# Kernel tuning notes

Measured on AMD Instinct MI355X. Metric: run time of the kernel, lower is better.

The kernel has to match this reference:

```python
import jax, jax.numpy as jnp
import numpy as np

B, S, D, H, DH, FF = 8, 512, 1024, 16, 64, 4096
NEG_MIN = jnp.finfo(jnp.float32).min


def setup_inputs() -> dict:
    key = jax.random.key(0)
    ks = jax.random.split(key, 12)
    sc = lambda d: d ** -0.5
    return {
        "x": jax.random.normal(ks[0], (B, S, D), jnp.float32),
        "mask": jnp.ones((B, S), jnp.float32),
        "special_attn": jax.nn.softmax(jax.random.normal(ks[1], (B, S, S), jnp.float32), axis=-1),
        "special_value": jax.random.normal(ks[2], (B, 1, S, DH), jnp.float32),
        "Wq": jax.random.normal(ks[3], (D, H * DH), jnp.float32) * sc(D),
        "bq": jnp.zeros((H * DH,), jnp.float32),
        "Wk": jax.random.normal(ks[4], (D, H * DH), jnp.float32) * sc(D),
        "bk": jnp.zeros((H * DH,), jnp.float32),
        "Wv": jax.random.normal(ks[5], (D, H * DH), jnp.float32) * sc(D),
        "bv": jnp.zeros((H * DH,), jnp.float32),
        "Wo": jax.random.normal(ks[6], ((H + 1) * DH, D), jnp.float32) * sc((H + 1) * DH),
        "bo": jnp.zeros((D,), jnp.float32),
        "ln1_g": jnp.ones((D,), jnp.float32),
        "ln1_b": jnp.zeros((D,), jnp.float32),
        "W1": jax.random.normal(ks[7], (D, FF), jnp.float32) * sc(D),
        "b1": jnp.zeros((FF,), jnp.float32),
        "W2": jax.random.normal(ks[8], (FF, D), jnp.float32) * sc(FF),
        "b2": jnp.zeros((D,), jnp.float32),
        "ln2_g": jnp.ones((D,), jnp.float32),
        "ln2_b": jnp.zeros((D,), jnp.float32),
    }


def _layer_norm(x, g, b, eps=1e-6):
    mu = jnp.mean(x, axis=-1, keepdims=True)
    var = jnp.mean(jnp.square(x - mu), axis=-1, keepdims=True)
    return (x - mu) * jax.lax.rsqrt(var + eps) * g + b


def _split_heads(t):  # [B,S,H*DH] -> [B,H,S,DH]
    return t.reshape(B, S, H, DH).transpose(0, 2, 1, 3)


def reference(x, mask, special_attn, special_value, Wq, bq, Wk, bk, Wv, bv,
              Wo, bo, ln1_g, ln1_b, W1, b1, W2, b2, ln2_g, ln2_b):
    # --- self-attention sublayer (pre-norm, residual) ---
    y = _layer_norm(x, ln1_g, ln1_b)
    q = _split_heads(y @ Wq + bq) * (DH ** -0.5)
    k = _split_heads(y @ Wk + bk)
    v = _split_heads(y @ Wv + bv)
    dot = jnp.einsum("bhqd,bhkd->bhqk", q, k)
    m = mask[:, None, None, :]  # [B,1,1,S]
    dot = dot * m + (1.0 - m) * NEG_MIN
    attn = jax.nn.softmax(dot, axis=-1)  # [B,H,S,S]
    # concat special attention map as an extra head; special values are PREPENDED
    attn = jnp.concatenate([attn, special_attn[:, None]], axis=1)   # [B,H+1,S,S]
    vals = jnp.concatenate([special_value, v], axis=1)              # [B,H+1,S,DH]
    heads = jnp.einsum("bhqk,bhkd->bhqd", attn, vals)               # [B,H+1,S,DH]
    combined = heads.transpose(0, 2, 1, 3).reshape(B, S, (H + 1) * DH)
    x = x + (combined @ Wo + bo)
    # --- FFN sublayer (pre-norm, residual, leaky_relu alpha=0.2) ---
    y = _layer_norm(x, ln2_g, ln2_b)
    h = jax.nn.leaky_relu(y @ W1 + b1, negative_slope=0.2)
    x = x + (h @ W2 + b2)
    return x
```

## Files before the change

### kernel.cpp

```cpp
#include <hip/hip_runtime.h>
#include <hip/hip_bf16.h>

#define BB 8
#define SS 512
#define DD 1024
#define HH 16
#define DHH 64
#define FFF 4096
#define MM (BB*SS)
#define HD (HH*DHH)
#define CD ((HH+1)*DHH)
#define QKV_LD 3072

#define NEG_MIN (-3.4028234663852886e38f)
#define FLT_MAX_ (3.402823466e+38f)

typedef __attribute__((ext_vector_type(8)))  __bf16 bf16x8;
typedef __attribute__((ext_vector_type(16))) float  f32x16;

__device__ __forceinline__ unsigned short bf16_rne(float x) {
    unsigned int u = __float_as_uint(x);
    u += 0x7FFFu + ((u >> 16) & 1u);
    return (unsigned short)(u >> 16);
}
__device__ __forceinline__ float bf16f(unsigned short h) {
    return __uint_as_float(((unsigned int)h) << 16);
}
__device__ __forceinline__ void split2(float x, unsigned short& h, unsigned short& l) {
    h = bf16_rne(x);
    l = bf16_rne(x - bf16f(h));
}

__global__ __launch_bounds__(256)
void ln_plane_kernel(const float* __restrict__ x, const float* __restrict__ g,
                     const float* __restrict__ bta,
                     unsigned short* __restrict__ oh, unsigned short* __restrict__ ol)
{
    const int row = blockIdx.x;
    const int tid = threadIdx.x;
    const float* xr = x + (size_t)row * DD;
    float4 xv = *(const float4*)(xr + tid * 4);
    float s  = xv.x + xv.y + xv.z + xv.w;
    float ss = xv.x*xv.x + xv.y*xv.y + xv.z*xv.z + xv.w*xv.w;
    #pragma unroll
    for (int off = 32; off > 0; off >>= 1) {
        s  += __shfl_down(s, off);
        ss += __shfl_down(ss, off);
    }
    __shared__ float red[8];
    const int wid = tid >> 6;
    if ((tid & 63) == 0) { red[wid*2] = s; red[wid*2+1] = ss; }
    __syncthreads();
    s  = red[0] + red[2] + red[4] + red[6];
    ss = red[1] + red[3] + red[5] + red[7];
    const float mu  = s * (1.0f / DD);
    const float var = ss * (1.0f / DD) - mu * mu;
    const float inv = 1.0f / sqrtf(var + 1e-6f);
    float4 gv = *(const float4*)(g + tid*4);
    float4 bv = *(const float4*)(bta + tid*4);
    float o0 = (xv.x - mu) * inv * gv.x + bv.x;
    float o1 = (xv.y - mu) * inv * gv.y + bv.y;
    float o2 = (xv.z - mu) * inv * gv.z + bv.z;
    float o3 = (xv.w - mu) * inv * gv.w + bv.w;
    ushort4 h4, l4;
    split2(o0, h4.x, l4.x); split2(o1, h4.y, l4.y);
    split2(o2, h4.z, l4.z); split2(o3, h4.w, l4.w);
    *(ushort4*)&oh[(size_t)row * DD + tid*4] = h4;
    *(ushort4*)&ol[(size_t)row * DD + tid*4] = l4;
}

template<bool QKV, bool HAS_RES, bool LEAKY, bool OUTP, int NT>
__global__ __launch_bounds__(256)
void gemm_mfma(const unsigned short* __restrict__ Ahi,
               const unsigned short* __restrict__ Alo,
               const float* __restrict__ B0, const float* __restrict__ B1,
               const float* __restrict__ B2,
               const float* __restrict__ bias0, const float* __restrict__ bias1,
               const float* __restrict__ bias2,
               const float* __restrict__ res, float* __restrict__ Cf,
               unsigned short* __restrict__ Chi, unsigned short* __restrict__ Clo,
               int K, int lda, int ldb, int ldc)
{
    static_assert(NT == 64 || NT == 128, "");
    constexpr int NF    = NT / 64;
    constexpr int BFRAG = NT / 32;
    constexpr int KG    = 256 / NT;
    constexpr int KPT   = 32 / KG;

    __shared__ unsigned short Ah[4096];
    __shared__ unsigned short Al[4096];
    __shared__ unsigned short Bh[BFRAG * 2 * 64 * 8];
    __shared__ unsigned short Bl[BFRAG * 2 * 64 * 8];

    const int tid = threadIdx.x;
    const int bm  = blockIdx.y;
    int bn = blockIdx.x;

    const float* Bw   = B0;
    const float* bias = bias0;
    float scale = 1.0f;
    if (QKV) {
        const int sel = bn >> 3;
        Bw   = (sel == 0) ? B0 : (sel == 1 ? B1 : B2);
        bias = (sel == 0) ? bias0 : (sel == 1 ? bias1 : bias2);
        scale = (sel == 0) ? 0.125f : 1.0f;
        bn &= 7;
    }

    const int wid  = tid >> 6, lane = tid & 63;
    const int wr   = wid >> 1, wc = wid & 1;
    const int lr   = lane & 31, kb = lane >> 5;

    f32x16 acc[2][NF];
    #pragma unroll
    for (int i = 0; i < 2; i++)
        #pragma unroll
        for (int j = 0; j < NF; j++)
            #pragma unroll
            for (int r = 0; r < 16; r++) acc[i][j][r] = 0.f;

    const int ar = tid >> 1, ao = (tid & 1) * 2;
    const unsigned short* Ahp = Ahi + (size_t)(bm*128 + ar) * lda + ao*8;
    const unsigned short* Alp = Alo + (size_t)(bm*128 + ar) * lda + ao*8;
    const int aidx0 = (((ao    >>1)*4 + (ar>>5))*64 + (ar & 31) + 32*( ao     & 1)) * 8;
    const int aidx1 = ((((ao+1)>>1)*4 + (ar>>5))*64 + (ar & 31) + 32*((ao+1) & 1)) * 8;
    const int nn = tid % NT, kg = tid / NT;
    const float* Bptr = Bw + (size_t)(kg*KPT) * ldb + bn*NT + nn;

    uint4 pah0, pah1, pal0, pal1;
    float pb[KPT];

    pah0 = *(const uint4*)(Ahp);
    pah1 = *(const uint4*)(Ahp + 8);
    pal0 = *(const uint4*)(Alp);
    pal1 = *(const uint4*)(Alp + 8);
    #pragma unroll
    for (int j = 0; j < KPT; ++j) pb[j] = Bptr[(size_t)j * ldb];

    for (int k0 = 0; k0 < K; k0 += 32) {
        *(uint4*)&Ah[aidx0] = pah0;
        *(uint4*)&Ah[aidx1] = pah1;
        *(uint4*)&Al[aidx0] = pal0;
        *(uint4*)&Al[aidx1] = pal1;
        #pragma unroll
        for (int c = 0; c < KPT/8; ++c) {
            unsigned int hw[4], lw[4];
            #pragma unroll
            for (int p = 0; p < 4; ++p) {
                unsigned short h0, l0, h1, l1;
                split2(pb[c*8 + 2*p],     h0, l0);
                split2(pb[c*8 + 2*p + 1], h1, l1);
                hw[p] = (unsigned int)h0 | ((unsigned int)h1 << 16);
                lw[p] = (unsigned int)l0 | ((unsigned int)l1 << 16);
            }
            const int k    = kg*KPT + c*8;
            const int base = (((k>>4)*BFRAG + (nn>>5))*64 + (nn & 31) + 32*((k>>3)&1))*8;
            *(uint4*)&Bh[base] = make_uint4(hw[0], hw[1], hw[2], hw[3]);
            *(uint4*)&Bl[base] = make_uint4(lw[0], lw[1], lw[2], lw[3]);
        }
        __syncthreads();

        const int kn = (k0 + 32 < K) ? (k0 + 32) : 0;
        pah0 = *(const uint4*)(Ahp + kn);
        pah1 = *(const uint4*)(Ahp + kn + 8);
        pal0 = *(const uint4*)(Alp + kn);
        pal1 = *(const uint4*)(Alp + kn + 8);
        #pragma unroll
        for (int j = 0; j < KPT; ++j) pb[j] = Bptr[(size_t)(kn + j) * ldb];

        #pragma unroll
        for (int ks = 0; ks < 2; ++ks) {
            bf16x8 ah[2], al2[2], bh2[NF], bl2[NF];
            #pragma unroll
            for (int mf = 0; mf < 2; ++mf) {
                const int idx = ((ks*4 + wr*2 + mf)*64 + lane) * 8;
                ah[mf]  = *(const bf16x8*)&Ah[idx];
                al2[mf] = *(const bf16x8*)&Al[idx];
            }
            #pragma unroll
            for (int nf = 0; nf < NF; ++nf) {
                const int idx = ((ks*BFRAG + wc*NF + nf)*64 + lane) * 8;
                bh2[nf] = *(const bf16x8*)&Bh[idx];
                bl2[nf] = *(const bf16x8*)&Bl[idx];
            }
            #pragma unroll
            for (int mf = 0; mf < 2; ++mf)
                #pragma unroll
                for (int nf = 0; nf < NF; ++nf) {
                    acc[mf][nf] = __builtin_amdgcn_mfma_f32_32x32x16_bf16(ah[mf],  bh2[nf], acc[mf][nf], 0, 0, 0);
                    acc[mf][nf] = __builtin_amdgcn_mfma_f32_32x32x16_bf16(ah[mf],  bl2[nf], acc[mf][nf], 0, 0, 0);
                    acc[mf][nf] = __builtin_amdgcn_mfma_f32_32x32x16_bf16(al2[mf], bh2[nf], acc[mf][nf], 0, 0, 0);
                }
        }
        __syncthreads();
    }

    #pragma unroll
    for (int mf = 0; mf < 2; ++mf)
        #pragma unroll
        for (int nf = 0; nf < NF; ++nf) {
            const int gcol = blockIdx.x*NT + wc*(32*NF) + nf*32 + lr;
            const float bsv = bias[bn*NT + wc*(32*NF) + nf*32 + lr];
            #pragma unroll
            for (int r = 0; r < 16; ++r) {
                const int grow = bm*128 + wr*64 + mf*32 + kb*4 + (r & 3) + 8*(r >> 2);
                float o = (acc[mf][nf][r] + bsv) * scale;
                if (HAS_RES) o += res[(size_t)grow * ldc + gcol];
                if (LEAKY)   o = o > 0.f ? o : 0.2f * o;
                if (OUTP) {
                    unsigned short h, l;
                    split2(o, h, l);
                    Chi[(size_t)grow * ldc + gcol] = h;
                    Clo[(size_t)grow * ldc + gcol] = l;
                } else {
                    Cf[(size_t)grow * ldc + gcol] = o;
                }
            }
        }
}

__global__ __launch_bounds__(256)
void attn_kernel(const float* __restrict__ qkv, const float* __restrict__ mask,
                 const float* __restrict__ sattn, const float* __restrict__ sval,
                 unsigned short* __restrict__ combh, unsigned short* __restrict__ combl)
{
    __shared__ float QsT[64][64];
    __shared__ float KT [64][64];
    __shared__ float Vs [64][64];
    const int tid = threadIdx.x;
    const int tx = tid & 15, ty = tid >> 4;
    const int qt = blockIdx.x, hh = blockIdx.y, b = blockIdx.z;
    const bool special = (hh == HH);

    const int li  = tid >> 2;
    const int ld0 = (tid & 3) * 16;

    if (!special) {
        const float* qbase = qkv + ((size_t)(b*SS + qt*64 + li)) * QKV_LD + hh*DHH;
        #pragma unroll
        for (int u = 0; u < 4; u++) {
            float4 t = *(const float4*)(qbase + ld0 + u*4);
            QsT[ld0+u*4+0][li] = t.x; QsT[ld0+u*4+1][li] = t.y;
            QsT[ld0+u*4+2][li] = t.z; QsT[ld0+u*4+3][li] = t.w;
        }
    }

    float m_i[4], l_i[4], oacc[4][4];
    #pragma unroll
    for (int r = 0; r < 4; r++) {
        m_i[r] = -FLT_MAX_;
        l_i[r] = special ? 1.f : 0.f;
        #pragma unroll
        for (int c = 0; c < 4; c++) oacc[r][c] = 0.f;
    }

    for (int kt = 0; kt < 8; ++kt) {
        __syncthreads();
        if (!special) {
            const float* kbase = qkv + ((size_t)(b*SS + kt*64 + li)) * QKV_LD + HD + hh*DHH;
            #pragma unroll
            for (int u = 0; u < 4; u++) {
                float4 t = *(const float4*)(kbase + ld0 + u*4);
                KT[ld0+u*4+0][li] = t.x; KT[ld0+u*4+1][li] = t.y;
                KT[ld0+u*4+2][li] = t.z; KT[ld0+u*4+3][li] = t.w;
            }
        } else {
            const float* pbase = sattn + ((size_t)b*SS + qt*64 + li) * SS + kt*64;
            #pragma unroll
            for (int u = 0; u < 4; u++) {
                float4 t = *(const float4*)(pbase + ld0 + u*4);
                KT[ld0+u*4+0][li] = t.x; KT[ld0+u*4+1][li] = t.y;
                KT[ld0+u*4+2][li] = t.z; KT[ld0+u*4+3][li] = t.w;
            }
        }
        {
            const float* vbase = (hh == 0)
                ? (sval + ((size_t)b*SS + kt*64 + li) * DHH)
                : (qkv + ((size_t)(b*SS + kt*64 + li)) * QKV_LD + 2*HD + (hh-1)*DHH);
            #pragma unroll
            for (int u = 0; u < 4; u++) {
                float4 t = *(const float4*)(vbase + ld0 + u*4);
                *(float4*)&Vs[li][ld0 + u*4] = t;
            }
        }
        __syncthreads();

        if (!special) {
            float sc[4][4];
            #pragma unroll
            for (int r = 0; r < 4; r++)
                #pragma unroll
                for (int c = 0; c < 4; c++) sc[r][c] = 0.f;
            #pragma unroll 8
            for (int d = 0; d < 64; ++d) {
                float4 qa = *(const float4*)&QsT[d][ty*4];
                float4 kb = *(const float4*)&KT[d][tx*4];
                float av[4] = {qa.x, qa.y, qa.z, qa.w};
                float bv[4] = {kb.x, kb.y, kb.z, kb.w};
                #pragma unroll
                for (int r = 0; r < 4; r++)
                    #pragma unroll
                    for (int c = 0; c < 4; c++)
                        sc[r][c] = fmaf(av[r], bv[c], sc[r][c]);
            }
            #pragma unroll
            for (int c = 0; c < 4; c++) {
                const float mk = mask[b*SS + kt*64 + tx*4 + c];
                const float add = (1.0f - mk) * NEG_MIN;
                #pragma unroll
                for (int r = 0; r < 4; r++)
                    sc[r][c] = sc[r][c] * mk + add;
            }
            float p[4][4];
            #pragma unroll
            for (int r = 0; r < 4; r++) {
                float rm = fmaxf(fmaxf(sc[r][0], sc[r][1]), fmaxf(sc[r][2], sc[r][3]));
                #pragma unroll
                for (int off = 1; off < 16; off <<= 1)
                    rm = fmaxf(rm, __shfl_xor(rm, off));
                const float m_new = fmaxf(m_i[r], rm);
                const float corr  = __expf(m_i[r] - m_new);
                float rs = 0.f;
                #pragma unroll
                for (int c = 0; c < 4; c++) {
                    p[r][c] = __expf(sc[r][c] - m_new);
                    rs += p[r][c];
                }
                #pragma unroll
                for (int off = 1; off < 16; off <<= 1)
                    rs += __shfl_xor(rs, off);
                l_i[r] = l_i[r] * corr + rs;
                m_i[r] = m_new;
                #pragma unroll
                for (int c = 0; c < 4; c++) oacc[r][c] *= corr;
            }
            __syncthreads();
            #pragma unroll
            for (int r = 0; r < 4; r++)
                #pragma unroll
                for (int c = 0; c < 4; c++)
                    KT[tx*4+c][ty*4+r] = p[r][c];
            __syncthreads();
        }
        #pragma unroll 8
        for (int j = 0; j < 64; ++j) {
            float4 pa = *(const float4*)&KT[j][ty*4];
            float4 vb = *(const float4*)&Vs[j][tx*4];
            float av[4] = {pa.x, pa.y, pa.z, pa.w};
            float bv[4] = {vb.x, vb.y, vb.z, vb.w};
            #pragma unroll
            for (int r = 0; r < 4; r++)
                #pragma unroll
                for (int c = 0; c < 4; c++)
                    oacc[r][c] = fmaf(av[r], bv[c], oacc[r][c]);
        }
    }
    #pragma unroll
    for (int r = 0; r < 4; r++) {
        const size_t row = (size_t)(b*SS + qt*64 + ty*4 + r);
        const float invl = 1.0f / l_i[r];
        ushort4 h4, l4;
        split2(oacc[r][0]*invl, h4.x, l4.x);
        split2(oacc[r][1]*invl, h4.y, l4.y);
        split2(oacc[r][2]*invl, h4.z, l4.z);
        split2(oacc[r][3]*invl, h4.w, l4.w);
        *(ushort4*)&combh[row * CD + hh*DHH + tx*4] = h4;
        *(ushort4*)&combl[row * CD + hh*DHH + tx*4] = l4;
    }
}

extern "C" void kernel_launch(void* const* d_in, const int* in_sizes, int n_in,
                              void* d_out, int out_size, void* d_ws, size_t ws_size,
                              hipStream_t stream)
{
    const float* x     = (const float*)d_in[0];
    const float* mask  = (const float*)d_in[1];
    const float* sattn = (const float*)d_in[2];
    const float* sval  = (const float*)d_in[3];
    const float* Wq    = (const float*)d_in[4];
    const float* bq    = (const float*)d_in[5];
    const float* Wk    = (const float*)d_in[6];
    const float* bk    = (const float*)d_in[7];
    const float* Wv    = (const float*)d_in[8];
    const float* bv    = (const float*)d_in[9];
    const float* Wo    = (const float*)d_in[10];
    const float* bo    = (const float*)d_in[11];
    const float* ln1g  = (const float*)d_in[12];
    const float* ln1b  = (const float*)d_in[13];
    const float* W1    = (const float*)d_in[14];
    const float* b1    = (const float*)d_in[15];
    const float* W2    = (const float*)d_in[16];
    const float* b2    = (const float*)d_in[17];
    const float* ln2g  = (const float*)d_in[18];
    const float* ln2b  = (const float*)d_in[19];

    char* wsb = (char*)d_ws;
    unsigned short* yh    = (unsigned short*)(wsb);
    unsigned short* yl    = (unsigned short*)(wsb + 8388608);
    float*          qkv   = (float*)         (wsb + 16777216);
    unsigned short* hhp   = (unsigned short*)(wsb);
    unsigned short* hlp   = (unsigned short*)(wsb + 33554432);
    unsigned short* combh = (unsigned short*)(wsb + 67108864);
    unsigned short* combl = (unsigned short*)(wsb + 76021760);
    float*          x2    = (float*)         (wsb + 84934656);
    unsigned short* y2h   = (unsigned short*)(wsb + 101711872);
    unsigned short* y2l   = (unsigned short*)(wsb + 110100480);

    const dim3 blk(256);

    ln_plane_kernel<<<MM, blk, 0, stream>>>(x, ln1g, ln1b, yh, yl);

    gemm_mfma<true,false,false,false,128><<<dim3(24, 32), blk, 0, stream>>>(
        yh, yl, Wq, Wk, Wv, bq, bk, bv,
        nullptr, qkv, nullptr, nullptr, DD, DD, DD, QKV_LD);

    attn_kernel<<<dim3(SS/64, HH+1, BB), blk, 0, stream>>>(qkv, mask, sattn, sval, combh, combl);

    gemm_mfma<false,true,false,false,64><<<dim3(16, 32), blk, 0, stream>>>(
        combh, combl, Wo, nullptr, nullptr, bo, nullptr, nullptr,
        x, x2, nullptr, nullptr, CD, CD, DD, DD);

    ln_plane_kernel<<<MM, blk, 0, stream>>>(x2, ln2g, ln2b, y2h, y2l);

    gemm_mfma<false,false,true,true,128><<<dim3(32, 32), blk, 0, stream>>>(
        y2h, y2l, W1, nullptr, nullptr, b1, nullptr, nullptr,
        nullptr, nullptr, hhp, hlp, DD, DD, FFF, FFF);

    gemm_mfma<false,true,false,false,64><<<dim3(16, 32), blk, 0, stream>>>(
        hhp, hlp, W2, nullptr, nullptr, b2, nullptr, nullptr,
        x2, (float*)d_out, nullptr, nullptr, FFF, FFF, DD, DD);
}
```

Before: 753.0 us.

## Rewrite attention kernel with bf16 split MFMA and 128-row query tiles

Replaces the scalar FP32 flash-attention kernel with one that uses 32x32x16 bf16 MFMA instructions. Q and K are split into hi/lo bf16 pairs (three products) and V into hi/lo (two products), which keeps near-FP32 accuracy, while the probabilities are rounded to a single bf16. K, V and P are staged in LDS with a swizzled layout, and each block now covers 128 query rows. The aim is to move the QK^T and PV matmuls off the vector ALUs. In exchange it rounds the probabilities and the special attention map to bf16, and it halves the number of blocks in the grid.

```diff
diff --git a/kernel.cpp b/kernel.cpp
--- a/kernel.cpp
+++ b/kernel.cpp
@@ -220,153 +220,199 @@
 }
 
 __global__ __launch_bounds__(256)
-void attn_kernel(const float* __restrict__ qkv, const float* __restrict__ mask,
-                 const float* __restrict__ sattn, const float* __restrict__ sval,
-                 unsigned short* __restrict__ combh, unsigned short* __restrict__ combl)
+void attn_mfma(const float* __restrict__ qkv, const float* __restrict__ mask,
+               const float* __restrict__ sattn, const float* __restrict__ sval,
+               unsigned short* __restrict__ combh, unsigned short* __restrict__ combl)
 {
-    __shared__ float QsT[64][64];
-    __shared__ float KT [64][64];
-    __shared__ float Vs [64][64];
+    __shared__ unsigned short KP[8192];
+    __shared__ unsigned short Vh[4096], Vl[4096];
+    __shared__ float msk[SS];
+
     const int tid = threadIdx.x;
-    const int tx = tid & 15, ty = tid >> 4;
+    const int w = tid >> 6, l = tid & 63, q = l & 31, lh = l >> 5;
     const int qt = blockIdx.x, hh = blockIdx.y, b = blockIdx.z;
     const bool special = (hh == HH);
-
-    const int li  = tid >> 2;
-    const int ld0 = (tid & 3) * 16;
-
+    const int swzl = l ^ ((l >> 3) & 7);
+
+    msk[tid]       = mask[b*SS + tid];
+    msk[tid + 256] = mask[b*SS + tid + 256];
+
+    union U8 { bf16x8 v; unsigned short s[8]; };
+
+    bf16x8 qfh[4], qfl[4];
     if (!special) {
-        const float* qbase = qkv + ((size_t)(b*SS + qt*64 + li)) * QKV_LD + hh*DHH;
-        #pragma unroll
-        for (int u = 0; u < 4; u++) {
-            float4 t = *(const float4*)(qbase + ld0 + u*4);
-            QsT[ld0+u*4+0][li] = t.x; QsT[ld0+u*4+1][li] = t.y;
-            QsT[ld0+u*4+2][li] = t.z; QsT[ld0+u*4+3][li] = t.w;
+        const float* qp = qkv + ((size_t)(b*SS + qt*128 + w*32 + q))*QKV_LD + hh*DHH + lh*8;
+        #pragma unroll
+        for (int ks = 0; ks < 4; ++ks) {
+            float4 a  = *(const float4*)(qp + ks*16);
+            float4 c2 = *(const float4*)(qp + ks*16 + 4);
+            U8 Hf, Lf;
+            split2(a.x,  Hf.s[0], Lf.s[0]); split2(a.y,  Hf.s[1], Lf.s[1]);
+            split2(a.z,  Hf.s[2], Lf.s[2]); split2(a.w,  Hf.s[3], Lf.s[3]);
+            split2(c2.x, Hf.s[4], Lf.s[4]); split2(c2.y, Hf.s[5], Lf.s[5]);
+            split2(c2.z, Hf.s[6], Lf.s[6]); split2(c2.w, Hf.s[7], Lf.s[7]);
+            qfh[ks] = Hf.v; qfl[ks] = Lf.v;
         }
     }
 
-    float m_i[4], l_i[4], oacc[4][4];
-    #pragma unroll
-    for (int r = 0; r < 4; r++) {
-        m_i[r] = -FLT_MAX_;
-        l_i[r] = special ? 1.f : 0.f;
-        #pragma unroll
-        for (int c = 0; c < 4; c++) oacc[r][c] = 0.f;
-    }
+    f32x16 ot0, ot1;
+    #pragma unroll
+    for (int r = 0; r < 16; ++r) { ot0[r] = 0.f; ot1[r] = 0.f; }
+    float m_i  = -FLT_MAX_;
+    float l_acc = special ? 1.f : 0.f;
+
+    const int skey = tid >> 2;
+    const int sd0  = (tid & 3) * 16;
 
     for (int kt = 0; kt < 8; ++kt) {
         __syncthreads();
+
+        {
+            const float* vrow = (hh == 0)
+                ? (sval + ((size_t)(b*SS + kt*64 + skey))*DHH + sd0)
+                : (qkv + ((size_t)(b*SS + kt*64 + skey))*QKV_LD + 2*HD + (hh-1)*DHH + sd0);
+            #pragma unroll
+            for (int c = 0; c < 4; ++c) {
+                float4 t4 = *(const float4*)(vrow + c*4);
+                float vv[4] = {t4.x, t4.y, t4.z, t4.w};
+                #pragma unroll
+                for (int j2 = 0; j2 < 4; ++j2) {
+                    const int d = sd0 + c*4 + j2;
+                    unsigned short hsv, lsv; split2(vv[j2], hsv, lsv);
+                    const int ur   = (d & 31) + 32*((skey >> 3) & 1);
+                    const int unit = ((d >> 5)*4 + (skey >> 4))*64 + (ur ^ ((ur >> 3) & 7));
+                    Vh[unit*8 + (skey & 7)] = hsv;
+                    Vl[unit*8 + (skey & 7)] = lsv;
+                }
+            }
+        }
         if (!special) {
-            const float* kbase = qkv + ((size_t)(b*SS + kt*64 + li)) * QKV_LD + HD + hh*DHH;
-            #pragma unroll
-            for (int u = 0; u < 4; u++) {
-                float4 t = *(const float4*)(kbase + ld0 + u*4);
-                KT[ld0+u*4+0][li] = t.x; KT[ld0+u*4+1][li] = t.y;
-                KT[ld0+u*4+2][li] = t.z; KT[ld0+u*4+3][li] = t.w;
+            const float* krow = qkv + ((size_t)(b*SS + kt*64 + skey))*QKV_LD + HD + hh*DHH + sd0;
+            #pragma unroll
+            for (int c = 0; c < 4; ++c) {
+                float4 t4 = *(const float4*)(krow + c*4);
+                unsigned short hs[4], ls[4];
+                split2(t4.x, hs[0], ls[0]); split2(t4.y, hs[1], ls[1]);
+                split2(t4.z, hs[2], ls[2]); split2(t4.w, hs[3], ls[3]);
+                #pragma unroll
+                for (int pp = 0; pp < 2; ++pp) {
+                    const int d = sd0 + c*4 + pp*2;
+                    const unsigned int ph = (unsigned int)hs[pp*2] | ((unsigned int)hs[pp*2+1] << 16);
+                    const unsigned int pl = (unsigned int)ls[pp*2] | ((unsigned int)ls[pp*2+1] << 16);
+                    const int ur   = (skey & 31) + 32*((d >> 3) & 1);
+                    const int unit = ((skey >> 5)*4 + (d >> 4))*64 + (ur ^ ((ur >> 3) & 7));
+                    *(unsigned int*)&KP[unit*8 + (d & 7)]        = ph;
+                    *(unsigned int*)&KP[4096 + unit*8 + (d & 7)] = pl;
+                }
             }
         } else {
-            const float* pbase = sattn + ((size_t)b*SS + qt*64 + li) * SS + kt*64;
-            #pragma unroll
-            for (int u = 0; u < 4; u++) {
-                float4 t = *(const float4*)(pbase + ld0 + u*4);
-                KT[ld0+u*4+0][li] = t.x; KT[ld0+u*4+1][li] = t.y;
-                KT[ld0+u*4+2][li] = t.z; KT[ld0+u*4+3][li] = t.w;
-            }
-        }
-        {
-            const float* vbase = (hh == 0)
-                ? (sval + ((size_t)b*SS + kt*64 + li) * DHH)
-                : (qkv + ((size_t)(b*SS + kt*64 + li)) * QKV_LD + 2*HD + (hh-1)*DHH);
-            #pragma unroll
-            for (int u = 0; u < 4; u++) {
-                float4 t = *(const float4*)(vbase + ld0 + u*4);
-                *(float4*)&Vs[li][ld0 + u*4] = t;
+            #pragma unroll
+            for (int i2 = 0; i2 < 4; ++i2) {
+                const int ug = i2*256 + tid;
+                const int wq = ug >> 8, ks = (ug >> 6) & 3, usw = ug & 63;
+                const int lr2 = usw ^ ((usw >> 3) & 7);
+                const int qq = lr2 & 31, kh = lr2 >> 5;
+                const float* pp = sattn + ((size_t)(b*SS + qt*128 + wq*32 + qq))*SS
+                                + kt*64 + ks*16 + kh*8;
+                float4 a  = *(const float4*)pp;
+                float4 c2 = *(const float4*)(pp + 4);
+                U8 P8;
+                P8.s[0]=bf16_rne(a.x);  P8.s[1]=bf16_rne(a.y);
+                P8.s[2]=bf16_rne(a.z);  P8.s[3]=bf16_rne(a.w);
+                P8.s[4]=bf16_rne(c2.x); P8.s[5]=bf16_rne(c2.y);
+                P8.s[6]=bf16_rne(c2.z); P8.s[7]=bf16_rne(c2.w);
+                *(bf16x8*)&KP[ug*8] = P8.v;
             }
         }
         __syncthreads();
 
         if (!special) {
-            float sc[4][4];
-            #pragma unroll
-            for (int r = 0; r < 4; r++)
+            f32x16 st0, st1;
+            #pragma unroll
+            for (int r = 0; r < 16; ++r) { st0[r] = 0.f; st1[r] = 0.f; }
+            #pragma unroll
+            for (int ks = 0; ks < 4; ++ks) {
+                bf16x8 k0h = *(const bf16x8*)&KP[((    ks)*64 + swzl)*8];
+                bf16x8 k0l = *(const bf16x8*)&KP[4096 + ((    ks)*64 + swzl)*8];
+                bf16x8 k1h = *(const bf16x8*)&KP[((4 + ks)*64 + swzl)*8];
+                bf16x8 k1l = *(const bf16x8*)&KP[4096 + ((4 + ks)*64 + swzl)*8];
+                st0 = __builtin_amdgcn_mfma_f32_32x32x16_bf16(k0h, qfh[ks], st0, 0, 0, 0);
+                st0 = __builtin_amdgcn_mfma_f32_32x32x16_bf16(k0h, qfl[ks], st0, 0, 0, 0);
+                st0 = __builtin_amdgcn_mfma_f32_32x32x16_bf16(k0l, qfh[ks], st0, 0, 0, 0);
+                st1 = __builtin_amdgcn_mfma_f32_32x32x16_bf16(k1h, qfh[ks], st1, 0, 0, 0);
+                st1 = __builtin_amdgcn_mfma_f32_32x32x16_bf16(k1h, qfl[ks], st1, 0, 0, 0);
+                st1 = __builtin_amdgcn_mfma_f32_32x32x16_bf16(k1l, qfh[ks], st1, 0, 0, 0);
+            }
+            float pmax = -FLT_MAX_;
+            #pragma unroll
+            for (int r = 0; r < 16; ++r) {
+                const int kl0 = (r & 3) + 8*(r >> 2) + 4*lh;
+                const float mv0 = msk[kt*64 + kl0];
+                const float mv1 = msk[kt*64 + 32 + kl0];
+                st0[r] = st0[r]*mv0 + (1.f - mv0)*NEG_MIN;
+                st1[r] = st1[r]*mv1 + (1.f - mv1)*NEG_MIN;
+                pmax = fmaxf(pmax, fmaxf(st0[r], st1[r]));
+            }
+            pmax = fmaxf(pmax, __shfl_xor(pmax, 32));
+            const float m_new = fmaxf(m_i, pmax);
+            const float corr  = __expf(m_i - m_new);
+            float rs = 0.f;
+            #pragma unroll
+            for (int r = 0; r < 16; ++r) {
+                st0[r] = __expf(st0[r] - m_new);
+                st1[r] = __expf(st1[r] - m_new);
+                rs += st0[r] + st1[r];
+            }
+            rs += __shfl_xor(rs, 32);
+            l_acc = l_acc*corr + rs;
+            m_i = m_new;
+            #pragma unroll
+            for (int r = 0; r < 16; ++r) { ot0[r] *= corr; ot1[r] *= corr; }
+
+            __syncthreads();
+            #pragma unroll
+            for (int t2 = 0; t2 < 2; ++t2)
                 #pragma unroll
-                for (int c = 0; c < 4; c++) sc[r][c] = 0.f;
-            #pragma unroll 8
-            for (int d = 0; d < 64; ++d) {
-                float4 qa = *(const float4*)&QsT[d][ty*4];
-                float4 kb = *(const float4*)&KT[d][tx*4];
-                float av[4] = {qa.x, qa.y, qa.z, qa.w};
-                float bv[4] = {kb.x, kb.y, kb.z, kb.w};
-                #pragma unroll
-                for (int r = 0; r < 4; r++)
-                    #pragma unroll
-                    for (int c = 0; c < 4; c++)
-                        sc[r][c] = fmaf(av[r], bv[c], sc[r][c]);
-            }
-            #pragma unroll
-            for (int c = 0; c < 4; c++) {
-                const float mk = mask[b*SS + kt*64 + tx*4 + c];
-                const float add = (1.0f - mk) * NEG_MIN;
-                #pragma unroll
-                for (int r = 0; r < 4; r++)
-                    sc[r][c] = sc[r][c] * mk + add;
-            }
-            float p[4][4];
-            #pragma unroll
-            for (int r = 0; r < 4; r++) {
-                float rm = fmaxf(fmaxf(sc[r][0], sc[r][1]), fmaxf(sc[r][2], sc[r][3]));
-                #pragma unroll
-                for (int off = 1; off < 16; off <<= 1)
-                    rm = fmaxf(rm, __shfl_xor(rm, off));
-                const float m_new = fmaxf(m_i[r], rm);
-                const float corr  = __expf(m_i[r] - m_new);
-                float rs = 0.f;
-                #pragma unroll
-                for (int c = 0; c < 4; c++) {
-                    p[r][c] = __expf(sc[r][c] - m_new);
-                    rs += p[r][c];
+                for (int rr = 0; rr < 16; rr += 2) {
+                    const int Kk = t2*32 + (rr & 3) + 8*(rr >> 2) + 4*lh;
+                    const int ks = Kk >> 4, kh = (Kk >> 3) & 1, e = Kk & 7;
+                    const int ur = q + 32*kh;
+                    const int unit = (w*4 + ks)*64 + (ur ^ ((ur >> 3) & 7));
+                    const float p0 = t2 ? st1[rr]     : st0[rr];
+                    const float p1 = t2 ? st1[rr + 1] : st0[rr + 1];
+                    const unsigned int pk = (unsigned int)bf16_rne(p0)
+                                          | ((unsigned int)bf16_rne(p1) << 16);
+                    *(unsigned int*)&KP[unit*8 + e] = pk;
                 }
-                #pragma unroll
-                for (int off = 1; off < 16; off <<= 1)
-                    rs += __shfl_xor(rs, off);
-                l_i[r] = l_i[r] * corr + rs;
-                m_i[r] = m_new;
-                #pragma unroll
-                for (int c = 0; c < 4; c++) oacc[r][c] *= corr;
-            }
             __syncthreads();
-            #pragma unroll
-            for (int r = 0; r < 4; r++)
-                #pragma unroll
-                for (int c = 0; c < 4; c++)
-                    KT[tx*4+c][ty*4+r] = p[r][c];
-            __syncthreads();
-        }
-        #pragma unroll 8
-        for (int j = 0; j < 64; ++j) {
-            float4 pa = *(const float4*)&KT[j][ty*4];
-            float4 vb = *(const float4*)&Vs[j][tx*4];
-            float av[4] = {pa.x, pa.y, pa.z, pa.w};
-            float bv[4] = {vb.x, vb.y, vb.z, vb.w};
-            #pragma unroll
-            for (int r = 0; r < 4; r++)
-                #pragma unroll
-                for (int c = 0; c < 4; c++)
-                    oacc[r][c] = fmaf(av[r], bv[c], oacc[r][c]);
+        }
+
+        #pragma unroll
+        for (int ks = 0; ks < 4; ++ks) {
+            bf16x8 pf  = *(const bf16x8*)&KP[((w*4 + ks)*64 + swzl)*8];
+            bf16x8 v0h = *(const bf16x8*)&Vh[((    ks)*64 + swzl)*8];
+            bf16x8 v0l = *(const bf16x8*)&Vl[((    ks)*64 + swzl)*8];
+            bf16x8 v1h = *(const bf16x8*)&Vh[((4 + ks)*64 + swzl)*8];
+            bf16x8 v1l = *(const bf16x8*)&Vl[((4 + ks)*64 + swzl)*8];
+            ot0 = __builtin_amdgcn_mfma_f32_32x32x16_bf16(v0h, pf, ot0, 0, 0, 0);
+            ot0 = __builtin_amdgcn_mfma_f32_32x32x16_bf16(v0l, pf, ot0, 0, 0, 0);
+            ot1 = __builtin_amdgcn_mfma_f32_32x32x16_bf16(v1h, pf, ot1, 0, 0, 0);
+            ot1 = __builtin_amdgcn_mfma_f32_32x32x16_bf16(v1l, pf, ot1, 0, 0, 0);
         }
     }
-    #pragma unroll
-    for (int r = 0; r < 4; r++) {
-        const size_t row = (size_t)(b*SS + qt*64 + ty*4 + r);
-        const float invl = 1.0f / l_i[r];
-        ushort4 h4, l4;
-        split2(oacc[r][0]*invl, h4.x, l4.x);
-        split2(oacc[r][1]*invl, h4.y, l4.y);
-        split2(oacc[r][2]*invl, h4.z, l4.z);
-        split2(oacc[r][3]*invl, h4.w, l4.w);
-        *(ushort4*)&combh[row * CD + hh*DHH + tx*4] = h4;
-        *(ushort4*)&combl[row * CD + hh*DHH + tx*4] = l4;
-    }
+
+    const float invl = 1.f / l_acc;
+    const size_t row = (size_t)(b*SS + qt*128 + w*32 + q);
+    #pragma unroll
+    for (int dt = 0; dt < 2; ++dt)
+        #pragma unroll
+        for (int r = 0; r < 16; ++r) {
+            const int d = dt*32 + (r & 3) + 8*(r >> 2) + 4*lh;
+            const float v = (dt ? ot1[r] : ot0[r]) * invl;
+            unsigned short hv, lv; split2(v, hv, lv);
+            combh[row*CD + hh*DHH + d] = hv;
+            combl[row*CD + hh*DHH + d] = lv;
+        }
 }
 
 extern "C" void kernel_launch(void* const* d_in, const int* in_sizes, int n_in,
@@ -414,7 +460,7 @@
         yh, yl, Wq, Wk, Wv, bq, bk, bv,
         nullptr, qkv, nullptr, nullptr, DD, DD, DD, QKV_LD);
 
-    attn_kernel<<<dim3(SS/64, HH+1, BB), blk, 0, stream>>>(qkv, mask, sattn, sval, combh, combl);
+    attn_mfma<<<dim3(SS/128, HH+1, BB), blk, 0, stream>>>(qkv, mask, sattn, sval, combh, combl);
 
     gemm_mfma<false,true,false,false,64><<<dim3(16, 32), blk, 0, stream>>>(
         combh, combl, Wo, nullptr, nullptr, bo, nullptr, nullptr,
```

Result: faster. 614.7 us (-18.4%).
